# Kernel optimization log

Hardware: AMD Instinct MI355X
Metric: run time of the kernel (lower is better)

## Reference

```python
import jax, jax.numpy as jnp
import numpy as np


def _lstm_scan(x_seq, W, U, b):
    # x_seq: [T, in_dim]; Keras gate order i, f, g(c), o; sigmoid/tanh activations.
    units = W.shape[1] // 4
    xz = x_seq @ W + b  # [T, 4*units], precompute input contribution

    def step(carry, xz_t):
        h, c = carry
        z = xz_t + h @ U
        i, f, g, o = jnp.split(z, 4)
        i = jax.nn.sigmoid(i)
        f = jax.nn.sigmoid(f)
        g = jnp.tanh(g)
        o = jax.nn.sigmoid(o)
        c_new = f * c + i * g
        h_new = o * jnp.tanh(c_new)
        return (h_new, c_new), h_new

    h0 = jnp.zeros((units,), dtype=x_seq.dtype)
    c0 = jnp.zeros((units,), dtype=x_seq.dtype)
    (_, _), hs = jax.lax.scan(step, (h0, c0), xz)
    return hs  # [T, units]


def setup_inputs() -> dict:
    key = jax.random.key(0)
    ks = jax.random.split(key, 6)
    var_num, g_dim, d, vocab = 256, 1024, 512, 32000
    s = lambda fi, fo: (2.0 / (fi + fo)) ** 0.5
    return {
        "context": jax.random.normal(ks[0], (var_num, g_dim), jnp.float32),
        "Wm": jax.random.normal(ks[1], (g_dim, d), jnp.float32) * s(g_dim, d),
        "bm": jnp.zeros((d,), jnp.float32),
        "W": jax.random.normal(ks[2], (d, 4 * d), jnp.float32) * s(d, 4 * d),
        "U": jax.random.normal(ks[3], (d, 4 * d), jnp.float32) * s(d, 4 * d),
        "b": jnp.zeros((4 * d,), jnp.float32),
        "Wl": jax.random.normal(ks[4], (d, vocab), jnp.float32) * s(d, vocab),
        "bl": jnp.zeros((vocab,), jnp.float32),
        "max_subtoken_len": 8,
    }


def reference(context, Wm, bm, W, U, b, Wl, bl, max_subtoken_len):
    # Dense merge of func/graph embedding (cat_func_g_emb branch)
    merged = context @ Wm + bm  # [var_num, d]
    var_num = merged.shape[0]
    # Original loop feeds the SAME [1, var_num, d] sequence through the LSTM
    # max_subtoken_len times, carrying (h, c) across iterations => one long
    # scan over the tiled sequence of length S * var_num.
    x_seq = jnp.tile(merged, (max_subtoken_len, 1))  # [S*var_num, d]
    hs = _lstm_scan(x_seq, W, U, b)  # [S*var_num, units]
    hs = hs.reshape(max_subtoken_len, var_num, -1)  # [S, var_num, units]
    logits = jnp.einsum("svd,dk->svk", hs, Wl) + bl  # [S, var_num, vocab]
    return jnp.transpose(logits, (1, 0, 2))  # [var_num, S, vocab]
```

## Files before the change

### kernel.cpp

```cpp
#include <hip/hip_runtime.h>
#include <stdint.h>

#define D 512
#define T 2048
#define VOCAB 32000
#define NWG 16

typedef __attribute__((ext_vector_type(8))) short short8;
typedef __attribute__((ext_vector_type(4))) float f32x4;
typedef __attribute__((ext_vector_type(8))) unsigned short u16x8;

__device__ __forceinline__ float fast_rcp(float x) { return __builtin_amdgcn_rcpf(x); }
__device__ __forceinline__ float sigm(float x) { return fast_rcp(1.0f + __expf(-x)); }
__device__ __forceinline__ float tanh_fast(float x) {
  float e = __expf(2.0f * x);
  return 1.0f - 2.0f * fast_rcp(e + 1.0f);
}
__device__ __forceinline__ unsigned short f2bf(float f) {
  unsigned u = __float_as_uint(f);
  unsigned r = u + 0x7fffu + ((u >> 16) & 1u);
  return (unsigned short)(r >> 16);
}

__global__ __launch_bounds__(512) void prep_kernel(
    const float* __restrict__ ctx, const float* __restrict__ Wm,
    const float* __restrict__ bm, const float* __restrict__ W,
    const float* __restrict__ b, float* __restrict__ xz)
{
  __shared__ float ctx_s[4][1024];
  __shared__ float mg_s[4][512];
  const int tid = threadIdx.x;
  const int r0 = blockIdx.x * 4;

  for (int i = tid; i < 1024; i += 512) {
    int rr = i >> 8, c4 = (i & 255) * 4;
    *(float4*)&ctx_s[rr][c4] = *(const float4*)&ctx[(size_t)(r0 + rr) * 1024 + c4];
  }
  __syncthreads();
  {
    const int rr = tid >> 7, cg = (tid & 127) * 4;
    float a0 = bm[cg], a1 = bm[cg + 1], a2 = bm[cg + 2], a3 = bm[cg + 3];
    for (int k = 0; k < 1024; k += 4) {
      float4 cv = *(float4*)&ctx_s[rr][k];
      #pragma unroll
      for (int kk = 0; kk < 4; kk++) {
        float cc = (kk == 0) ? cv.x : (kk == 1) ? cv.y : (kk == 2) ? cv.z : cv.w;
        float4 wv = *(const float4*)&Wm[(size_t)(k + kk) * 512 + cg];
        a0 += cc * wv.x; a1 += cc * wv.y; a2 += cc * wv.z; a3 += cc * wv.w;
      }
    }
    *(float4*)&mg_s[rr][cg] = make_float4(a0, a1, a2, a3);
  }
  __syncthreads();
  {
    const int rr = tid >> 7, cg = (tid & 127) * 16;
    float acc[16];
    #pragma unroll
    for (int c = 0; c < 16; c++) acc[c] = b[cg + c];
    for (int k = 0; k < 512; k += 4) {
      float4 mv = *(float4*)&mg_s[rr][k];
      #pragma unroll
      for (int kk = 0; kk < 4; kk++) {
        float cc = (kk == 0) ? mv.x : (kk == 1) ? mv.y : (kk == 2) ? mv.z : mv.w;
        #pragma unroll
        for (int c4 = 0; c4 < 4; c4++) {
          float4 wv = *(const float4*)&W[(size_t)(k + kk) * 2048 + cg + c4 * 4];
          acc[c4 * 4 + 0] += cc * wv.x; acc[c4 * 4 + 1] += cc * wv.y;
          acc[c4 * 4 + 2] += cc * wv.z; acc[c4 * 4 + 3] += cc * wv.w;
        }
      }
    }
    #pragma unroll
    for (int c4 = 0; c4 < 4; c4++)
      *(float4*)&xz[(size_t)(r0 + rr) * 2048 + cg + c4 * 4] =
          make_float4(acc[c4 * 4], acc[c4 * 4 + 1], acc[c4 * 4 + 2], acc[c4 * 4 + 3]);
  }
}

__global__ __launch_bounds__(256) void wl_convert_kernel(
    const float* __restrict__ Wl, unsigned short* __restrict__ Wlt)
{
  const int c = blockIdx.x * 256 + threadIdx.x;
  for (int k8 = 0; k8 < 64; k8++) {
    u16x8 v;
    #pragma unroll
    for (int e = 0; e < 8; e++)
      v[e] = f2bf(Wl[(size_t)(k8 * 8 + e) * VOCAB + c]);
    *(u16x8*)&Wlt[(size_t)c * 512 + k8 * 8] = v;
  }
}

__global__ __launch_bounds__(512, 2) void lstm_kernel(
    const float* __restrict__ xz, const float* __restrict__ U,
    uint64_t* __restrict__ hb, unsigned short* __restrict__ hs)
{
  __shared__ float h_lds[512];
  __shared__ float z_lds[128];
  const int tid = threadIdx.x;
  const int wg = blockIdx.x;
  const int rb = tid & 31;
  const int cb = tid >> 5;
  const int gate = cb >> 2;
  const int gcol0 = gate * 512 + wg * 32 + (cb & 3) * 8;

  float u[16][8];
  #pragma unroll
  for (int e = 0; e < 16; e++) {
    const float* up = &U[(size_t)(rb + 32 * e) * 2048 + gcol0];
    float4 w0 = *(const float4*)up;
    float4 w1 = *(const float4*)(up + 4);
    u[e][0] = w0.x; u[e][1] = w0.y; u[e][2] = w0.z; u[e][3] = w0.w;
    u[e][4] = w1.x; u[e][5] = w1.y; u[e][6] = w1.z; u[e][7] = w1.w;
  }

  float creg = 0.0f;

  for (int t = 0; t < T; t++) {
    float xzv0, xzv1, xzv2, xzv3;
    if (tid < 32) {
      const float* xp = &xz[(size_t)(t & 255) * 2048 + wg * 32 + tid];
      xzv0 = xp[0]; xzv1 = xp[512]; xzv2 = xp[1024]; xzv3 = xp[1536];
    }
    {
      const uint64_t* hw = hb + (size_t)(t & 1) * 512 + tid;
      uint64_t wv;
      for (;;) {
        wv = __hip_atomic_load(hw, __ATOMIC_RELAXED, __HIP_MEMORY_SCOPE_AGENT);
        if ((unsigned)(wv >> 32) == (unsigned)t) break;
      }
      h_lds[tid] = __uint_as_float((unsigned)wv);
    }
    __syncthreads();
    float hv[16];
    #pragma unroll
    for (int e = 0; e < 16; e++) hv[e] = h_lds[rb + 32 * e];
    float zp[8];
    #pragma unroll
    for (int c = 0; c < 8; c++) zp[c] = 0.0f;
    #pragma unroll
    for (int e = 0; e < 16; e++) {
      #pragma unroll
      for (int c = 0; c < 8; c++) zp[c] += hv[e] * u[e][c];
    }
    #pragma unroll
    for (int m = 1; m < 32; m <<= 1) {
      #pragma unroll
      for (int c = 0; c < 8; c++) zp[c] += __shfl_xor(zp[c], m, 64);
    }
    if (rb == 0) {
      *(float4*)&z_lds[cb * 8]     = make_float4(zp[0], zp[1], zp[2], zp[3]);
      *(float4*)&z_lds[cb * 8 + 4] = make_float4(zp[4], zp[5], zp[6], zp[7]);
    }
    __syncthreads();
    if (tid < 32) {
      float zi = z_lds[tid]       + xzv0;
      float zf = z_lds[32 + tid]  + xzv1;
      float zg = z_lds[64 + tid]  + xzv2;
      float zo = z_lds[96 + tid]  + xzv3;
      float ig = sigm(zi), fg = sigm(zf), gg = tanh_fast(zg), og = sigm(zo);
      creg = fg * creg + ig * gg;
      float h = og * tanh_fast(creg);
      hs[(size_t)t * 512 + wg * 32 + tid] = f2bf(h);
      uint64_t pk = ((uint64_t)(unsigned)(t + 1) << 32) | (uint64_t)__float_as_uint(h);
      __hip_atomic_store(&hb[(size_t)((t + 1) & 1) * 512 + wg * 32 + tid], pk,
                         __ATOMIC_RELAXED, __HIP_MEMORY_SCOPE_AGENT);
    }
  }
}

__global__ __launch_bounds__(256) void logits_kernel(
    const unsigned short* __restrict__ hs, const unsigned short* __restrict__ Wlt,
    const float* __restrict__ bl, float* __restrict__ out)
{
  __shared__ unsigned short As[128][40];
  __shared__ unsigned short Bs[128][40];
  const int tid = threadIdx.x;
  const int bx = blockIdx.x, by = blockIdx.y;
  const int lane = tid & 63, w = tid >> 6;
  const int wr = w >> 1, wc = w & 1;

  f32x4 acc[4][4];
  #pragma unroll
  for (int i = 0; i < 4; i++) {
    #pragma unroll
    for (int j = 0; j < 4; j++) acc[i][j] = (f32x4){0.0f, 0.0f, 0.0f, 0.0f};
  }

  for (int kk = 0; kk < 512; kk += 32) {
    #pragma unroll
    for (int i = 0; i < 2; i++) {
      int chunk = tid * 2 + i;
      int r = chunk >> 2, c8 = (chunk & 3) * 8;
      *(uint4*)&As[r][c8] = *(const uint4*)&hs[(size_t)(by * 128 + r) * 512 + kk + c8];
      *(uint4*)&Bs[r][c8] = *(const uint4*)&Wlt[(size_t)(bx * 128 + r) * 512 + kk + c8];
    }
    __syncthreads();
    short8 af[4], bf[4];
    #pragma unroll
    for (int fr = 0; fr < 4; fr++)
      af[fr] = *(const short8*)&As[wr * 64 + fr * 16 + (lane & 15)][(lane >> 4) * 8];
    #pragma unroll
    for (int fc = 0; fc < 4; fc++)
      bf[fc] = *(const short8*)&Bs[wc * 64 + fc * 16 + (lane & 15)][(lane >> 4) * 8];
    #pragma unroll
    for (int fr = 0; fr < 4; fr++) {
      #pragma unroll
      for (int fc = 0; fc < 4; fc++)
        acc[fr][fc] = __builtin_amdgcn_mfma_f32_16x16x32_bf16(af[fr], bf[fc], acc[fr][fc], 0, 0, 0);
    }
    __syncthreads();
  }

  #pragma unroll
  for (int fc = 0; fc < 4; fc++) {
    int col = bx * 128 + wc * 64 + fc * 16 + (lane & 15);
    float blv = bl[col];
    #pragma unroll
    for (int fr = 0; fr < 4; fr++) {
      int row0 = by * 128 + wr * 64 + fr * 16 + (lane >> 4) * 4;
      #pragma unroll
      for (int j = 0; j < 4; j++) {
        int row = row0 + j;
        int orow = (row & 255) * 8 + (row >> 8);
        out[(size_t)orow * VOCAB + col] = acc[fr][fc][j] + blv;
      }
    }
  }
}

extern "C" void kernel_launch(void* const* d_in, const int* in_sizes, int n_in,
                              void* d_out, int out_size, void* d_ws, size_t ws_size,
                              hipStream_t stream)
{
  const float* ctx = (const float*)d_in[0];
  const float* Wm  = (const float*)d_in[1];
  const float* bm  = (const float*)d_in[2];
  const float* W   = (const float*)d_in[3];
  const float* U   = (const float*)d_in[4];
  const float* b   = (const float*)d_in[5];
  const float* Wl  = (const float*)d_in[6];
  const float* bl  = (const float*)d_in[7];
  float* out = (float*)d_out;

  char* ws = (char*)d_ws;
  uint64_t* hb        = (uint64_t*)ws;
  float* xz           = (float*)(ws + 65536);
  unsigned short* hs  = (unsigned short*)(ws + 65536 + (1 << 21));
  unsigned short* Wlt = (unsigned short*)(ws + 65536 + (2 << 21));

  hipMemsetAsync(hb, 0, 8192, stream);
  prep_kernel<<<dim3(64), dim3(512), 0, stream>>>(ctx, Wm, bm, W, b, xz);
  wl_convert_kernel<<<dim3(125), dim3(256), 0, stream>>>(Wl, Wlt);

  void* args[] = { (void*)&xz, (void*)&U, (void*)&hb, (void*)&hs };
  hipLaunchCooperativeKernel((void*)lstm_kernel, dim3(NWG), dim3(512), args, 0, stream);

  logits_kernel<<<dim3(250, 16), dim3(256), 0, stream>>>(hs, Wlt, bl, out);
}
```

Baseline: 4.874 ms.

## Remap LSTM columns so each warp owns full gate set, dropping z_lds reduction stage

Each 32-lane group now holds all four gate columns for two hidden units, so the lane that finishes the shuffle reduction computes the cell update directly. This removes the z_lds exchange and the narrow tid<32 activation phase from the serial recurrence. The h poll loop now keeps four atomic loads in flight, so polling latency is overlapped. Occupancy hint drops to one block per CU, and U loads become strided scalar loads, which only affects setup.

```diff
diff --git a/kernel.cpp b/kernel.cpp
--- a/kernel.cpp
+++ b/kernel.cpp
@@ -20,6 +20,9 @@
   unsigned u = __float_as_uint(f);
   unsigned r = u + 0x7fffu + ((u >> 16) & 1u);
   return (unsigned short)(r >> 16);
+}
+__device__ __forceinline__ uint64_t AL(const uint64_t* p) {
+  return __hip_atomic_load(p, __ATOMIC_RELAXED, __HIP_MEMORY_SCOPE_AGENT);
 }
 
 __global__ __launch_bounds__(512) void prep_kernel(
@@ -90,81 +93,95 @@
   }
 }
 
-__global__ __launch_bounds__(512, 2) void lstm_kernel(
+__global__ __launch_bounds__(512, 1) void lstm_kernel(
     const float* __restrict__ xz, const float* __restrict__ U,
     uint64_t* __restrict__ hb, unsigned short* __restrict__ hs)
 {
   __shared__ float h_lds[512];
-  __shared__ float z_lds[128];
   const int tid = threadIdx.x;
   const int wg = blockIdx.x;
   const int rb = tid & 31;
   const int cb = tid >> 5;
-  const int gate = cb >> 2;
-  const int gcol0 = gate * 512 + wg * 32 + (cb & 3) * 8;
+  const int u0 = wg * 32 + cb * 2;
+  const bool gl = (rb == 0);
 
   float u[16][8];
   #pragma unroll
   for (int e = 0; e < 16; e++) {
-    const float* up = &U[(size_t)(rb + 32 * e) * 2048 + gcol0];
-    float4 w0 = *(const float4*)up;
-    float4 w1 = *(const float4*)(up + 4);
-    u[e][0] = w0.x; u[e][1] = w0.y; u[e][2] = w0.z; u[e][3] = w0.w;
-    u[e][4] = w1.x; u[e][5] = w1.y; u[e][6] = w1.z; u[e][7] = w1.w;
-  }
-
-  float creg = 0.0f;
+    const float* up = &U[(size_t)(rb + 32 * e) * 2048 + u0];
+    #pragma unroll
+    for (int g = 0; g < 4; g++) {
+      u[e][g * 2]     = up[g * 512];
+      u[e][g * 2 + 1] = up[g * 512 + 1];
+    }
+  }
+  #pragma unroll
+  for (int e = 0; e < 16; e++) {
+    #pragma unroll
+    for (int c = 0; c < 8; c++) asm volatile("" : "+v"(u[e][c]));
+  }
+
+  float c0 = 0.0f, c1 = 0.0f;
 
   for (int t = 0; t < T; t++) {
-    float xzv0, xzv1, xzv2, xzv3;
-    if (tid < 32) {
-      const float* xp = &xz[(size_t)(t & 255) * 2048 + wg * 32 + tid];
-      xzv0 = xp[0]; xzv1 = xp[512]; xzv2 = xp[1024]; xzv3 = xp[1536];
+    float xv[8];
+    if (gl) {
+      const float* xp = &xz[(size_t)(t & 255) * 2048 + u0];
+      #pragma unroll
+      for (int g = 0; g < 4; g++) { xv[g * 2] = xp[g * 512]; xv[g * 2 + 1] = xp[g * 512 + 1]; }
     }
     {
-      const uint64_t* hw = hb + (size_t)(t & 1) * 512 + tid;
-      uint64_t wv;
+      const uint64_t* hw = hb + (size_t)((t & 1) << 9) + tid;
+      uint64_t v0 = AL(hw), v1 = AL(hw), v2 = AL(hw), v3 = AL(hw);
+      float hval;
       for (;;) {
-        wv = __hip_atomic_load(hw, __ATOMIC_RELAXED, __HIP_MEMORY_SCOPE_AGENT);
-        if ((unsigned)(wv >> 32) == (unsigned)t) break;
-      }
-      h_lds[tid] = __uint_as_float((unsigned)wv);
-    }
-    __syncthreads();
-    float hv[16];
-    #pragma unroll
-    for (int e = 0; e < 16; e++) hv[e] = h_lds[rb + 32 * e];
+        if ((unsigned)(v0 >> 32) == (unsigned)t) { hval = __uint_as_float((unsigned)v0); break; }
+        v0 = AL(hw);
+        if ((unsigned)(v1 >> 32) == (unsigned)t) { hval = __uint_as_float((unsigned)v1); break; }
+        v1 = AL(hw);
+        if ((unsigned)(v2 >> 32) == (unsigned)t) { hval = __uint_as_float((unsigned)v2); break; }
+        v2 = AL(hw);
+        if ((unsigned)(v3 >> 32) == (unsigned)t) { hval = __uint_as_float((unsigned)v3); break; }
+        v3 = AL(hw);
+      }
+      h_lds[tid] = hval;
+    }
+    __syncthreads();
+
     float zp[8];
     #pragma unroll
     for (int c = 0; c < 8; c++) zp[c] = 0.0f;
     #pragma unroll
     for (int e = 0; e < 16; e++) {
-      #pragma unroll
-      for (int c = 0; c < 8; c++) zp[c] += hv[e] * u[e][c];
+      float hv = h_lds[rb + 32 * e];
+      #pragma unroll
+      for (int c = 0; c < 8; c++) zp[c] = __builtin_fmaf(hv, u[e][c], zp[c]);
     }
     #pragma unroll
     for (int m = 1; m < 32; m <<= 1) {
       #pragma unroll
       for (int c = 0; c < 8; c++) zp[c] += __shfl_xor(zp[c], m, 64);
     }
-    if (rb == 0) {
-      *(float4*)&z_lds[cb * 8]     = make_float4(zp[0], zp[1], zp[2], zp[3]);
-      *(float4*)&z_lds[cb * 8 + 4] = make_float4(zp[4], zp[5], zp[6], zp[7]);
-    }
-    __syncthreads();
-    if (tid < 32) {
-      float zi = z_lds[tid]       + xzv0;
-      float zf = z_lds[32 + tid]  + xzv1;
-      float zg = z_lds[64 + tid]  + xzv2;
-      float zo = z_lds[96 + tid]  + xzv3;
-      float ig = sigm(zi), fg = sigm(zf), gg = tanh_fast(zg), og = sigm(zo);
-      creg = fg * creg + ig * gg;
-      float h = og * tanh_fast(creg);
-      hs[(size_t)t * 512 + wg * 32 + tid] = f2bf(h);
-      uint64_t pk = ((uint64_t)(unsigned)(t + 1) << 32) | (uint64_t)__float_as_uint(h);
-      __hip_atomic_store(&hb[(size_t)((t + 1) & 1) * 512 + wg * 32 + tid], pk,
+
+    if (gl) {
+      float i0 = sigm(zp[0] + xv[0]), i1 = sigm(zp[1] + xv[1]);
+      float f0 = sigm(zp[2] + xv[2]), f1 = sigm(zp[3] + xv[3]);
+      float g0 = tanh_fast(zp[4] + xv[4]), g1 = tanh_fast(zp[5] + xv[5]);
+      float o0 = sigm(zp[6] + xv[6]), o1 = sigm(zp[7] + xv[7]);
+      c0 = f0 * c0 + i0 * g0;
+      c1 = f1 * c1 + i1 * g1;
+      float h0 = o0 * tanh_fast(c0);
+      float h1 = o1 * tanh_fast(c1);
+      uint64_t tag = ((uint64_t)(unsigned)(t + 1)) << 32;
+      uint64_t* dst = hb + (size_t)(((t + 1) & 1) << 9) + u0;
+      __hip_atomic_store(dst,     tag | (uint64_t)__float_as_uint(h0),
                          __ATOMIC_RELAXED, __HIP_MEMORY_SCOPE_AGENT);
-    }
+      __hip_atomic_store(dst + 1, tag | (uint64_t)__float_as_uint(h1),
+                         __ATOMIC_RELAXED, __HIP_MEMORY_SCOPE_AGENT);
+      unsigned hp = (unsigned)f2bf(h0) | ((unsigned)f2bf(h1) << 16);
+      *(unsigned*)&hs[(size_t)t * 512 + u0] = hp;
+    }
+    __syncthreads();
   }
 }
 
```

Measured after the change: 6.183 ms. 26.9% more time.

## Pack recurrent weights as fp16 pairs and use fdot2 in LSTM step

Applied to the files above, without the earlier changes.

Adds a conversion kernel that packs U into fp16 pairs (row r and r+32 interleaved), so each LSTM thread holds half as many weight registers. The inner h·U product becomes v_dot2 fp16 instructions with fp32 accumulation, halving the FMA count on the serial per-timestep critical path. Asm barriers keep the packed weights resident in registers, and launch bounds drop to one block per CU. This trades recurrent-matmul precision (fp16 weights and fp16-rounded h) for lower per-step latency, and adds a small extra conversion kernel.

```diff
diff --git a/kernel.cpp b/kernel.cpp
--- a/kernel.cpp
+++ b/kernel.cpp
@@ -9,6 +9,7 @@
 typedef __attribute__((ext_vector_type(8))) short short8;
 typedef __attribute__((ext_vector_type(4))) float f32x4;
 typedef __attribute__((ext_vector_type(8))) unsigned short u16x8;
+typedef __attribute__((ext_vector_type(2))) __fp16 f16x2;
 
 __device__ __forceinline__ float fast_rcp(float x) { return __builtin_amdgcn_rcpf(x); }
 __device__ __forceinline__ float sigm(float x) { return fast_rcp(1.0f + __expf(-x)); }
@@ -21,6 +22,10 @@
   unsigned r = u + 0x7fffu + ((u >> 16) & 1u);
   return (unsigned short)(r >> 16);
 }
+__device__ __forceinline__ uint64_t AL(const uint64_t* p) {
+  return __hip_atomic_load(p, __ATOMIC_RELAXED, __HIP_MEMORY_SCOPE_AGENT);
+}
+union U32H2 { unsigned u; f16x2 h; };
 
 __global__ __launch_bounds__(512) void prep_kernel(
     const float* __restrict__ ctx, const float* __restrict__ Wm,
@@ -90,8 +95,30 @@
   }
 }
 
-__global__ __launch_bounds__(512, 2) void lstm_kernel(
-    const float* __restrict__ xz, const float* __restrict__ U,
+__global__ __launch_bounds__(256) void uconv_kernel(
+    const float* __restrict__ U, unsigned* __restrict__ Up)
+{
+  const int p = blockIdx.x;
+  const int c0 = threadIdx.x * 8;
+  const int r_lo = (p >> 5) * 64 + (p & 31);
+  const float* lo = &U[(size_t)r_lo * 2048 + c0];
+  const float* hi = &U[(size_t)(r_lo + 32) * 2048 + c0];
+  unsigned outv[8];
+  #pragma unroll
+  for (int c = 0; c < 8; c++) {
+    U32H2 w;
+    w.h[0] = (__fp16)lo[c];
+    w.h[1] = (__fp16)hi[c];
+    outv[c] = w.u;
+  }
+  #pragma unroll
+  for (int c4 = 0; c4 < 2; c4++)
+    *(uint4*)&Up[(size_t)p * 2048 + c0 + c4 * 4] =
+        make_uint4(outv[c4 * 4], outv[c4 * 4 + 1], outv[c4 * 4 + 2], outv[c4 * 4 + 3]);
+}
+
+__global__ __launch_bounds__(512, 1) void lstm_kernel(
+    const float* __restrict__ xz, const unsigned* __restrict__ Up,
     uint64_t* __restrict__ hb, unsigned short* __restrict__ hs)
 {
   __shared__ float h_lds[512];
@@ -103,44 +130,61 @@
   const int gate = cb >> 2;
   const int gcol0 = gate * 512 + wg * 32 + (cb & 3) * 8;
 
-  float u[16][8];
-  #pragma unroll
-  for (int e = 0; e < 16; e++) {
-    const float* up = &U[(size_t)(rb + 32 * e) * 2048 + gcol0];
-    float4 w0 = *(const float4*)up;
-    float4 w1 = *(const float4*)(up + 4);
-    u[e][0] = w0.x; u[e][1] = w0.y; u[e][2] = w0.z; u[e][3] = w0.w;
-    u[e][4] = w1.x; u[e][5] = w1.y; u[e][6] = w1.z; u[e][7] = w1.w;
+  uint4 uv[16];
+  #pragma unroll
+  for (int ep = 0; ep < 8; ep++) {
+    const unsigned* ap = &Up[(size_t)(ep * 32 + rb) * 2048 + gcol0];
+    asm volatile("global_load_dwordx4 %0, %1, off"
+                 : "=v"(uv[ep * 2]) : "v"(ap));
+    asm volatile("global_load_dwordx4 %0, %1, off offset:16"
+                 : "=v"(uv[ep * 2 + 1]) : "v"(ap));
+  }
+  asm volatile("s_waitcnt vmcnt(0)" ::: "memory");
+  unsigned u2[8][8];
+  #pragma unroll
+  for (int ep = 0; ep < 8; ep++) {
+    uint4 a = uv[ep * 2], b4 = uv[ep * 2 + 1];
+    u2[ep][0] = a.x; u2[ep][1] = a.y; u2[ep][2] = a.z; u2[ep][3] = a.w;
+    u2[ep][4] = b4.x; u2[ep][5] = b4.y; u2[ep][6] = b4.z; u2[ep][7] = b4.w;
   }
 
   float creg = 0.0f;
 
   for (int t = 0; t < T; t++) {
+    #pragma unroll
+    for (int ep = 0; ep < 8; ep++) {
+      #pragma unroll
+      for (int c = 0; c < 8; c++) asm volatile("" : "+v"(u2[ep][c]));
+    }
     float xzv0, xzv1, xzv2, xzv3;
     if (tid < 32) {
       const float* xp = &xz[(size_t)(t & 255) * 2048 + wg * 32 + tid];
       xzv0 = xp[0]; xzv1 = xp[512]; xzv2 = xp[1024]; xzv3 = xp[1536];
     }
     {
-      const uint64_t* hw = hb + (size_t)(t & 1) * 512 + tid;
+      const uint64_t* hw = hb + (size_t)((t & 1) << 9) + tid;
       uint64_t wv;
       for (;;) {
-        wv = __hip_atomic_load(hw, __ATOMIC_RELAXED, __HIP_MEMORY_SCOPE_AGENT);
+        wv = AL(hw);
         if ((unsigned)(wv >> 32) == (unsigned)t) break;
       }
       h_lds[tid] = __uint_as_float((unsigned)wv);
     }
     __syncthreads();
-    float hv[16];
-    #pragma unroll
-    for (int e = 0; e < 16; e++) hv[e] = h_lds[rb + 32 * e];
+
     float zp[8];
     #pragma unroll
     for (int c = 0; c < 8; c++) zp[c] = 0.0f;
     #pragma unroll
-    for (int e = 0; e < 16; e++) {
-      #pragma unroll
-      for (int c = 0; c < 8; c++) zp[c] += hv[e] * u[e][c];
+    for (int ep = 0; ep < 8; ep++) {
+      float hlo = h_lds[rb + 64 * ep];
+      float hhi = h_lds[rb + 64 * ep + 32];
+      f16x2 h2 = __builtin_amdgcn_cvt_pkrtz(hlo, hhi);
+      #pragma unroll
+      for (int c = 0; c < 8; c++) {
+        U32H2 w; w.u = u2[ep][c];
+        zp[c] = __builtin_amdgcn_fdot2(h2, w.h, zp[c], false);
+      }
     }
     #pragma unroll
     for (int m = 1; m < 32; m <<= 1) {
@@ -162,7 +206,7 @@
       float h = og * tanh_fast(creg);
       hs[(size_t)t * 512 + wg * 32 + tid] = f2bf(h);
       uint64_t pk = ((uint64_t)(unsigned)(t + 1) << 32) | (uint64_t)__float_as_uint(h);
-      __hip_atomic_store(&hb[(size_t)((t + 1) & 1) * 512 + wg * 32 + tid], pk,
+      __hip_atomic_store(&hb[(size_t)(((t + 1) & 1) << 9) + wg * 32 + tid], pk,
                          __ATOMIC_RELAXED, __HIP_MEMORY_SCOPE_AGENT);
     }
   }
@@ -246,13 +290,15 @@
   uint64_t* hb        = (uint64_t*)ws;
   float* xz           = (float*)(ws + 65536);
   unsigned short* hs  = (unsigned short*)(ws + 65536 + (1 << 21));
-  unsigned short* Wlt = (unsigned short*)(ws + 65536 + (2 << 21));
+  unsigned* Up        = (unsigned*)(ws + 65536 + (2 << 21));
+  unsigned short* Wlt = (unsigned short*)(ws + 65536 + (3 << 21));
 
   hipMemsetAsync(hb, 0, 8192, stream);
   prep_kernel<<<dim3(64), dim3(512), 0, stream>>>(ctx, Wm, bm, W, b, xz);
+  uconv_kernel<<<dim3(256), dim3(256), 0, stream>>>(U, Up);
   wl_convert_kernel<<<dim3(125), dim3(256), 0, stream>>>(Wl, Wlt);
 
-  void* args[] = { (void*)&xz, (void*)&U, (void*)&hb, (void*)&hs };
+  void* args[] = { (void*)&xz, (void*)&Up, (void*)&hb, (void*)&hs };
   hipLaunchCooperativeKernel((void*)lstm_kernel, dim3(NWG), dim3(512), args, 0, stream);
 
   logits_kernel<<<dim3(250, 16), dim3(256), 0, stream>>>(hs, Wlt, bl, out);
```

Result: slower. 5.109 ms (+4.8%).
